# Kernel tuning notes

Measured on AMD Instinct MI355X. Metric: run time of the kernel, lower is better.

## Reference

```python
import jax, jax.numpy as jnp
import numpy as np

N = 500_000
IN_FEAT = 128
HIDDEN = 128
OUT_FEAT = 128
CODE_DIM = 32
NUM_CODES = 256


def _linear_params(key, fan_in, fan_out):
    kw, kb = jax.random.split(key)
    bound = 1.0 / np.sqrt(fan_in)
    W = jax.random.uniform(kw, (fan_out, fan_in), jnp.float32, -bound, bound)
    b = jax.random.uniform(kb, (fan_out,), jnp.float32, -bound, bound)
    return W, b


def setup_inputs() -> dict:
    key = jax.random.key(0)
    ks = jax.random.split(key, 6)
    x = jax.random.normal(ks[0], (N, IN_FEAT), jnp.float32)
    W_down, b_down = _linear_params(ks[1], IN_FEAT, HIDDEN)
    W_pin, b_pin = _linear_params(ks[2], HIDDEN, CODE_DIM)      # VQ project_in 128->32
    codebook = jax.random.normal(ks[3], (NUM_CODES, CODE_DIM), jnp.float32)
    W_pout, b_pout = _linear_params(ks[4], CODE_DIM, HIDDEN)    # VQ project_out 32->128
    W_up, b_up = _linear_params(ks[5], HIDDEN, OUT_FEAT)
    return {"x": x, "W_down": W_down, "b_down": b_down,
            "W_pin": W_pin, "b_pin": b_pin, "codebook": codebook,
            "W_pout": W_pout, "b_pout": b_pout,
            "W_up": W_up, "b_up": b_up}


def reference(x, W_down, b_down, W_pin, b_pin, codebook, W_pout, b_pout, W_up, b_up):
    # down: Linear(128 -> 128)
    h = x @ W_down.T + b_down                                   # [N, 128]
    # VQ project_in: Linear(128 -> 32)
    z = h @ W_pin.T + b_pin                                     # [N, 32]
    # squared euclidean distance to codebook, argmin assignment
    d2 = (jnp.sum(z * z, axis=-1, keepdims=True)
          - 2.0 * (z @ codebook.T)
          + jnp.sum(codebook * codebook, axis=-1))              # [N, 256]
    indices = jnp.argmin(d2, axis=-1)                           # [N] int
    q = codebook[indices]                                       # gather [N, 32]
    # straight-through estimator
    q_ste = z + jax.lax.stop_gradient(q - z)
    # VQ project_out: Linear(32 -> 128)
    v = q_ste @ W_pout.T + b_pout                               # [N, 128]
    # up: Linear(128 -> 128), then clamp
    y = jnp.clip(v @ W_up.T + b_up, -1.0, 1.0)                  # [N, 128]
    # commitment_weight = 0 -> commit loss is exactly zero
    commit_loss = jnp.zeros((), x.dtype)
    return y, indices, commit_loss
```

## Files before the change

### kernel.cpp

```cpp
#include <hip/hip_runtime.h>


#define CODE_D 32
#define NUM_C  256
#define KCH    32
#define LSTR   36


__global__ void vq_prep1(const float* __restrict__ Wd, const float* __restrict__ bd,
                         const float* __restrict__ Wp, const float* __restrict__ bp,
                         const float* __restrict__ cb,
                         float* __restrict__ Wc, float* __restrict__ bc,
                         float* __restrict__ cbias) {
    const int t = threadIdx.x;
    for (int e = t; e < 32 * 128; e += 256) {
        const int j = e >> 7, k = e & 127;
        double s = 0.0;
        for (int m = 0; m < 128; ++m)
            s += (double)Wp[j * 128 + m] * (double)Wd[m * 128 + k];
        Wc[e] = (float)s;
    }
    if (t < 32) {
        double s = (double)bp[t];
        for (int m = 0; m < 128; ++m) s += (double)Wp[t * 128 + m] * (double)bd[m];
        bc[t] = (float)s;
    }
    {
        float s = 0.f;
        for (int d = 0; d < CODE_D; ++d) { float v = cb[t * CODE_D + d]; s += v * v; }
        cbias[t] = -0.5f * s;
    }
}

__global__ void vq_prep2(const float* __restrict__ cb, const float* __restrict__ Wpo,
                         const float* __restrict__ bpo, const float* __restrict__ Wu,
                         const float* __restrict__ bu, float* __restrict__ ytab) {
    __shared__ float v[128];
    const int c = blockIdx.x;
    const int t = threadIdx.x;
    float s = bpo[t];
    for (int d = 0; d < CODE_D; ++d) s += cb[c * CODE_D + d] * Wpo[t * CODE_D + d];
    v[t] = s;
    __syncthreads();
    float o = bu[t];
    for (int m = 0; m < 128; ++m) o += v[m] * Wu[t * 128 + m];
    o = fminf(fmaxf(o, -1.0f), 1.0f);
    ytab[c * 128 + t] = o;
}


__global__ __launch_bounds__(256, 4) void vq_main(
    const float* __restrict__ x,
    const float* __restrict__ Wc,
    const float* __restrict__ bc,
    const float* __restrict__ cb,
    const float* __restrict__ cbias,
    const float* __restrict__ ytab,
    float* __restrict__ y,
    float* __restrict__ idx_out,
    float* __restrict__ loss_out,
    int N) {
    __shared__ float lds[256 * LSTR];
    __shared__ int sidx[256];

    const int t = threadIdx.x;
    const int row0 = blockIdx.x * 256;
    const int myrow = row0 + t;

    float z[CODE_D];
#pragma unroll
    for (int j = 0; j < CODE_D; ++j) z[j] = bc[j];

    const int rr = t >> 3;
    const int qq = t & 7;
    for (int kc = 0; kc < 128; kc += KCH) {
#pragma unroll
        for (int i = 0; i < 8; ++i) {
            const int r = i * 32 + rr;
            const int grow = row0 + r;
            float4 v = make_float4(0.f, 0.f, 0.f, 0.f);
            if (grow < N)
                v = *reinterpret_cast<const float4*>(x + (size_t)grow * 128 + kc + qq * 4);
            *reinterpret_cast<float4*>(&lds[r * LSTR + qq * 4]) = v;
        }
        __syncthreads();
#pragma unroll
        for (int q = 0; q < KCH / 4; ++q) {
            const float4 xv = *reinterpret_cast<const float4*>(&lds[t * LSTR + q * 4]);
            const int kb = kc + q * 4;
#pragma unroll
            for (int j = 0; j < CODE_D; ++j) {
                const float* w = Wc + j * 128 + kb;
                z[j] += w[0] * xv.x + w[1] * xv.y + w[2] * xv.z + w[3] * xv.w;
            }
        }
        __syncthreads();
    }

    float best = -3.0e38f;
    int besti = 0;
#pragma unroll 4
    for (int c = 0; c < NUM_C; ++c) {
        const float* crow = cb + c * CODE_D;
        float s0 = 0.f, s1 = 0.f, s2 = 0.f, s3 = 0.f;
#pragma unroll
        for (int d = 0; d < CODE_D; d += 4) {
            s0 += crow[d + 0] * z[d + 0];
            s1 += crow[d + 1] * z[d + 1];
            s2 += crow[d + 2] * z[d + 2];
            s3 += crow[d + 3] * z[d + 3];
        }
        const float s = ((s0 + s1) + (s2 + s3)) + cbias[c];
        if (s > best) { best = s; besti = c; }
    }

    sidx[t] = besti;
    if (myrow < N) idx_out[myrow] = (float)besti;
    __syncthreads();

    const int rsub = t >> 5;
    const int c4 = t & 31;
#pragma unroll
    for (int i = 0; i < 32; ++i) {
        const int r = i * 8 + rsub;
        const int grow = row0 + r;
        if (grow < N) {
            const int ci = sidx[r];
            const float4 v = *reinterpret_cast<const float4*>(ytab + ci * 128 + c4 * 4);
            *reinterpret_cast<float4*>(y + (size_t)grow * 128 + c4 * 4) = v;
        }
    }

    if (blockIdx.x == 0 && t == 0) loss_out[0] = 0.0f;
}


extern "C" void kernel_launch(void* const* d_in, const int* in_sizes, int n_in,
                              void* d_out, int out_size, void* d_ws, size_t ws_size,
                              hipStream_t stream) {
    const float* x   = (const float*)d_in[0];
    const float* Wd  = (const float*)d_in[1];
    const float* bd  = (const float*)d_in[2];
    const float* Wp  = (const float*)d_in[3];
    const float* bp  = (const float*)d_in[4];
    const float* cb  = (const float*)d_in[5];
    const float* Wpo = (const float*)d_in[6];
    const float* bpo = (const float*)d_in[7];
    const float* Wu  = (const float*)d_in[8];
    const float* bu  = (const float*)d_in[9];

    const int N = in_sizes[0] / 128;

    float* ws    = (float*)d_ws;
    float* Wc    = ws;
    float* bc    = ws + 4096;
    float* cbias = ws + 4128;
    float* ytab  = ws + 4384;

    float* y    = (float*)d_out;
    float* idxf = y + (size_t)N * 128;
    float* loss = idxf + N;

    vq_prep1<<<1, 256, 0, stream>>>(Wd, bd, Wp, bp, cb, Wc, bc, cbias);
    vq_prep2<<<NUM_C, 128, 0, stream>>>(cb, Wpo, bpo, Wu, bu, ytab);

    const int blocks = (N + 255) / 256;
    vq_main<<<blocks, 256, 0, stream>>>(x, Wc, bc, cb, cbias, ytab, y, idxf, loss, N);
}
```

Measured before the change: 934.7 us.

## Parallelize weight-fold prep across blocks and load x rows directly

The single-block prep kernel that folds W_pin·W_down in double precision is spread over 18 blocks, one output chunk per block plus separate blocks for the bias and codebook norms. The main kernel drops the LDS staging of x tiles and the barriers around it; each thread now reads its own row straight from global memory with float4 loads. The launch-bounds occupancy hint goes from 4 to 6 blocks. Per-thread row reads are strided by 512 bytes across lanes, so coalescing is worse, traded for no LDS use and no syncs.

```diff
diff --git a/kernel.cpp b/kernel.cpp
--- a/kernel.cpp
+++ b/kernel.cpp
@@ -3,8 +3,6 @@
 
 #define CODE_D 32
 #define NUM_C  256
-#define KCH    32
-#define LSTR   36
 
 
 __global__ void vq_prep1(const float* __restrict__ Wd, const float* __restrict__ bd,
@@ -13,20 +11,26 @@
                          float* __restrict__ Wc, float* __restrict__ bc,
                          float* __restrict__ cbias) {
     const int t = threadIdx.x;
-    for (int e = t; e < 32 * 128; e += 256) {
+    const int b = blockIdx.x;
+    if (b < 16) {
+        const int e = b * 256 + t;
         const int j = e >> 7, k = e & 127;
-        double s = 0.0;
-        for (int m = 0; m < 128; ++m)
-            s += (double)Wp[j * 128 + m] * (double)Wd[m * 128 + k];
-        Wc[e] = (float)s;
-    }
-    if (t < 32) {
-        double s = (double)bp[t];
-        for (int m = 0; m < 128; ++m) s += (double)Wp[t * 128 + m] * (double)bd[m];
-        bc[t] = (float)s;
-    }
-    {
+        double s0 = 0.0, s1 = 0.0;
+#pragma unroll 8
+        for (int m = 0; m < 128; m += 2) {
+            s0 += (double)Wp[j * 128 + m]     * (double)Wd[(m) * 128 + k];
+            s1 += (double)Wp[j * 128 + m + 1] * (double)Wd[(m + 1) * 128 + k];
+        }
+        Wc[e] = (float)(s0 + s1);
+    } else if (b == 16) {
+        if (t < 32) {
+            double s = (double)bp[t];
+            for (int m = 0; m < 128; ++m) s += (double)Wp[t * 128 + m] * (double)bd[m];
+            bc[t] = (float)s;
+        }
+    } else {
         float s = 0.f;
+#pragma unroll
         for (int d = 0; d < CODE_D; ++d) { float v = cb[t * CODE_D + d]; s += v * v; }
         cbias[t] = -0.5f * s;
     }
@@ -49,7 +53,7 @@
 }
 
 
-__global__ __launch_bounds__(256, 4) void vq_main(
+__global__ __launch_bounds__(256, 6) void vq_main(
     const float* __restrict__ x,
     const float* __restrict__ Wc,
     const float* __restrict__ bc,
@@ -60,41 +64,27 @@
     float* __restrict__ idx_out,
     float* __restrict__ loss_out,
     int N) {
-    __shared__ float lds[256 * LSTR];
     __shared__ int sidx[256];
 
     const int t = threadIdx.x;
     const int row0 = blockIdx.x * 256;
     const int myrow = row0 + t;
+    const int rd = myrow < N ? myrow : (N - 1);
 
     float z[CODE_D];
 #pragma unroll
     for (int j = 0; j < CODE_D; ++j) z[j] = bc[j];
 
-    const int rr = t >> 3;
-    const int qq = t & 7;
-    for (int kc = 0; kc < 128; kc += KCH) {
+    const float* __restrict__ xr = x + (size_t)rd * 128;
 #pragma unroll
-        for (int i = 0; i < 8; ++i) {
-            const int r = i * 32 + rr;
-            const int grow = row0 + r;
-            float4 v = make_float4(0.f, 0.f, 0.f, 0.f);
-            if (grow < N)
-                v = *reinterpret_cast<const float4*>(x + (size_t)grow * 128 + kc + qq * 4);
-            *reinterpret_cast<float4*>(&lds[r * LSTR + qq * 4]) = v;
+    for (int q = 0; q < 32; ++q) {
+        const float4 xv = *reinterpret_cast<const float4*>(xr + q * 4);
+        const int kb = q * 4;
+#pragma unroll
+        for (int j = 0; j < CODE_D; ++j) {
+            const float* w = Wc + j * 128 + kb;
+            z[j] += w[0] * xv.x + w[1] * xv.y + w[2] * xv.z + w[3] * xv.w;
         }
-        __syncthreads();
-#pragma unroll
-        for (int q = 0; q < KCH / 4; ++q) {
-            const float4 xv = *reinterpret_cast<const float4*>(&lds[t * LSTR + q * 4]);
-            const int kb = kc + q * 4;
-#pragma unroll
-            for (int j = 0; j < CODE_D; ++j) {
-                const float* w = Wc + j * 128 + kb;
-                z[j] += w[0] * xv.x + w[1] * xv.y + w[2] * xv.z + w[3] * xv.w;
-            }
-        }
-        __syncthreads();
     }
 
     float best = -3.0e38f;
@@ -161,7 +151,7 @@
     float* idxf = y + (size_t)N * 128;
     float* loss = idxf + N;
 
-    vq_prep1<<<1, 256, 0, stream>>>(Wd, bd, Wp, bp, cb, Wc, bc, cbias);
+    vq_prep1<<<18, 256, 0, stream>>>(Wd, bd, Wp, bp, cb, Wc, bc, cbias);
     vq_prep2<<<NUM_C, 128, 0, stream>>>(cb, Wpo, bpo, Wu, bu, ytab);
 
     const int blocks = (N + 255) / 256;
```

Result: slower. 962.5 us (+3.0%).

## Pair adjacent threads to split projection and codebook search, stage codebook in LDS

Applied to the files above, without the earlier changes.

Each thread pair now shares two rows. For the projection, each lane computes half of the 32 code dimensions for both rows, and the halves are swapped via shuffles. For the argmin search, each lane scans half of the 256 codes for both rows, and the two partial winners are merged by shuffle. The codebook and its bias are copied into shared memory instead of being read through global/scalar loads. The prep kernel is split across 18 blocks instead of one serial block. This trades more registers and LDS reads per thread, and a slightly different tie-break order, for fewer redundant weight loads per row and better parallelism in setup.

```diff
diff --git a/kernel.cpp b/kernel.cpp
--- a/kernel.cpp
+++ b/kernel.cpp
@@ -13,20 +13,26 @@
                          float* __restrict__ Wc, float* __restrict__ bc,
                          float* __restrict__ cbias) {
     const int t = threadIdx.x;
-    for (int e = t; e < 32 * 128; e += 256) {
+    const int b = blockIdx.x;
+    if (b < 16) {
+        const int e = b * 256 + t;
         const int j = e >> 7, k = e & 127;
-        double s = 0.0;
-        for (int m = 0; m < 128; ++m)
-            s += (double)Wp[j * 128 + m] * (double)Wd[m * 128 + k];
-        Wc[e] = (float)s;
-    }
-    if (t < 32) {
-        double s = (double)bp[t];
-        for (int m = 0; m < 128; ++m) s += (double)Wp[t * 128 + m] * (double)bd[m];
-        bc[t] = (float)s;
-    }
-    {
+        double s0 = 0.0, s1 = 0.0;
+#pragma unroll 8
+        for (int m = 0; m < 128; m += 2) {
+            s0 += (double)Wp[j * 128 + m]     * (double)Wd[(m) * 128 + k];
+            s1 += (double)Wp[j * 128 + m + 1] * (double)Wd[(m + 1) * 128 + k];
+        }
+        Wc[e] = (float)(s0 + s1);
+    } else if (b == 16) {
+        if (t < 32) {
+            double s = (double)bp[t];
+            for (int m = 0; m < 128; ++m) s += (double)Wp[t * 128 + m] * (double)bd[m];
+            bc[t] = (float)s;
+        }
+    } else {
         float s = 0.f;
+#pragma unroll
         for (int d = 0; d < CODE_D; ++d) { float v = cb[t * CODE_D + d]; s += v * v; }
         cbias[t] = -0.5f * s;
     }
@@ -61,15 +67,21 @@
     float* __restrict__ loss_out,
     int N) {
     __shared__ float lds[256 * LSTR];
+    __shared__ float scb[NUM_C];
     __shared__ int sidx[256];
 
     const int t = threadIdx.x;
     const int row0 = blockIdx.x * 256;
     const int myrow = row0 + t;
 
-    float z[CODE_D];
-#pragma unroll
-    for (int j = 0; j < CODE_D; ++j) z[j] = bc[j];
+    const int tA = t & ~1;
+    const int tB = t | 1;
+    const bool oddlane = (t & 1);
+    const int jb = (t & 1) << 4;
+
+    float zA[16], zB[16];
+#pragma unroll
+    for (int j = 0; j < 16; ++j) { zA[j] = bc[jb + j]; zB[j] = zA[j]; }
 
     const int rr = t >> 3;
     const int qq = t & 7;
@@ -86,37 +98,72 @@
         __syncthreads();
 #pragma unroll
         for (int q = 0; q < KCH / 4; ++q) {
-            const float4 xv = *reinterpret_cast<const float4*>(&lds[t * LSTR + q * 4]);
+            const float4 xa = *reinterpret_cast<const float4*>(&lds[tA * LSTR + q * 4]);
+            const float4 xb = *reinterpret_cast<const float4*>(&lds[tB * LSTR + q * 4]);
             const int kb = kc + q * 4;
 #pragma unroll
-            for (int j = 0; j < CODE_D; ++j) {
-                const float* w = Wc + j * 128 + kb;
-                z[j] += w[0] * xv.x + w[1] * xv.y + w[2] * xv.z + w[3] * xv.w;
+            for (int j = 0; j < 16; ++j) {
+                const float* w = Wc + (jb + j) * 128 + kb;
+                zA[j] += w[0] * xa.x + w[1] * xa.y + w[2] * xa.z + w[3] * xa.w;
+                zB[j] += w[0] * xb.x + w[1] * xb.y + w[2] * xb.z + w[3] * xb.w;
             }
         }
         __syncthreads();
     }
 
-    float best = -3.0e38f;
-    int besti = 0;
-#pragma unroll 4
-    for (int c = 0; c < NUM_C; ++c) {
-        const float* crow = cb + c * CODE_D;
-        float s0 = 0.f, s1 = 0.f, s2 = 0.f, s3 = 0.f;
-#pragma unroll
-        for (int d = 0; d < CODE_D; d += 4) {
-            s0 += crow[d + 0] * z[d + 0];
-            s1 += crow[d + 1] * z[d + 1];
-            s2 += crow[d + 2] * z[d + 2];
-            s3 += crow[d + 3] * z[d + 3];
-        }
-        const float s = ((s0 + s1) + (s2 + s3)) + cbias[c];
-        if (s > best) { best = s; besti = c; }
-    }
-
-    sidx[t] = besti;
-    if (myrow < N) idx_out[myrow] = (float)besti;
+    float zfA[32], zfB[32];
+#pragma unroll
+    for (int j = 0; j < 16; ++j) {
+        const float p = __shfl_xor(zA[j], 1);
+        zfA[j]      = oddlane ? p     : zA[j];
+        zfA[j + 16] = oddlane ? zA[j] : p;
+    }
+#pragma unroll
+    for (int j = 0; j < 16; ++j) {
+        const float p = __shfl_xor(zB[j], 1);
+        zfB[j]      = oddlane ? p     : zB[j];
+        zfB[j + 16] = oddlane ? zB[j] : p;
+    }
+
+#pragma unroll
+    for (int i = 0; i < 8; ++i)
+        reinterpret_cast<float4*>(lds)[i * 256 + t] =
+            reinterpret_cast<const float4*>(cb)[i * 256 + t];
+    scb[t] = cbias[t];
     __syncthreads();
+
+    const int cbase = (t & 1) << 7;
+    float bestA = -3.0e38f, bestB = -3.0e38f;
+    int iA = 0, iB = 0;
+#pragma unroll 2
+    for (int i = 0; i < 128; ++i) {
+        const int c = cbase + i;
+        const float* crow = &lds[c * CODE_D];
+        float sA = scb[c];
+        float sB = sA;
+#pragma unroll
+        for (int d4 = 0; d4 < 8; ++d4) {
+            const float4 cv = *reinterpret_cast<const float4*>(crow + d4 * 4);
+            sA += cv.x * zfA[d4 * 4 + 0] + cv.y * zfA[d4 * 4 + 1]
+                + cv.z * zfA[d4 * 4 + 2] + cv.w * zfA[d4 * 4 + 3];
+            sB += cv.x * zfB[d4 * 4 + 0] + cv.y * zfB[d4 * 4 + 1]
+                + cv.z * zfB[d4 * 4 + 2] + cv.w * zfB[d4 * 4 + 3];
+        }
+        if (sA > bestA) { bestA = sA; iA = c; }
+        if (sB > bestB) { bestB = sB; iB = c; }
+    }
+
+    const float pBA = __shfl_xor(bestA, 1);
+    const int   pIA = __shfl_xor(iA, 1);
+    const float pBB = __shfl_xor(bestB, 1);
+    const int   pIB = __shfl_xor(iB, 1);
+    if (!oddlane) {
+        sidx[tA] = (pBA > bestA) ? pIA : iA;
+        sidx[tB] = (pBB > bestB) ? pIB : iB;
+    }
+    __syncthreads();
+
+    if (myrow < N) idx_out[myrow] = (float)sidx[t];
 
     const int rsub = t >> 5;
     const int c4 = t & 31;
@@ -161,7 +208,7 @@
     float* idxf = y + (size_t)N * 128;
     float* loss = idxf + N;
 
-    vq_prep1<<<1, 256, 0, stream>>>(Wd, bd, Wp, bp, cb, Wc, bc, cbias);
+    vq_prep1<<<18, 256, 0, stream>>>(Wd, bd, Wp, bp, cb, Wc, bc, cbias);
     vq_prep2<<<NUM_C, 128, 0, stream>>>(cb, Wpo, bpo, Wu, bu, ytab);
 
     const int blocks = (N + 255) / 256;
```

New measurement: 2.210 ms. 2.36x slower.
